# Kernel tuning notes

Hardware: AMD Instinct MI355X
Metric: run time of the kernel (lower is better)

Reference implementation:

```python
import jax, jax.numpy as jnp
from jax import lax
import numpy as np

N, CH_I, CH_H, CH_Q, K, IMSIZE = 128, 2, 150, 10, 16, 64
EPS = 1e-5


def _conv(x, w):
    # 3x3, stride 1, pad 1 == SAME; NCHW / OIHW
    return lax.conv_general_dilated(x, w, (1, 1), 'SAME',
                                    dimension_numbers=('NCHW', 'OIHW', 'NCHW'))


def _maxpool2(x):
    return lax.reduce_window(x, -jnp.inf, lax.max, (1, 1, 2, 2), (1, 1, 2, 2), 'VALID')


def _upsample2(x):
    n, c, h, w = x.shape
    # torch Upsample(scale_factor=2, mode='bilinear', align_corners=False)
    return jax.image.resize(x, (n, c, 2 * h, 2 * w), method='linear')


def _vi_loop(new_r, conv_q_ws, denom):
    # value-iteration recurrence: rv = cat([new_r, v]); q = conv_i(rv); v = max_c q; sum += v
    v0 = jnp.zeros_like(new_r[:, :1])

    def step(carry, w):
        v, s = carry
        rv = jnp.concatenate([new_r, v], axis=1)
        q = _conv(rv, w)
        v = jnp.max(q, axis=1, keepdims=True)
        return (v, s + v), None

    (_, s), _ = lax.scan(step, (v0, v0), conv_q_ws)
    return s / denom


def setup_inputs() -> dict:
    key = jax.random.key(0)
    ks = jax.random.split(key, 12)
    g = lambda k, shp, fan: jax.random.normal(k, shp, dtype=jnp.float32) * (1.0 / np.sqrt(fan))
    X = jax.random.normal(ks[0], (N, CH_I, IMSIZE, IMSIZE), dtype=jnp.float32)
    S1 = jax.random.randint(ks[1], (N,), 0, IMSIZE)
    S2 = jax.random.randint(ks[2], (N,), 0, IMSIZE)
    return {
        'X': X, 'S1': S1, 'S2': S2,
        'conv_h_w': g(ks[3], (CH_H, CH_I, 3, 3), CH_I * 9),
        'conv_r_w': g(ks[4], (1, CH_H, 3, 3), CH_H * 9),
        'conv_q_ws': g(ks[5], (K, CH_Q, 3, 3, 3), 3 * 9),
        'bn_gamma': jnp.ones((CH_Q,), jnp.float32),
        'bn_beta': jnp.zeros((CH_Q,), jnp.float32),
        'duel_w1': g(ks[6], (1, CH_Q), CH_Q),
        'duel_w2': g(ks[7], (8, CH_Q), CH_Q),
        'vi_conv_h_w': g(ks[8], (150, 2, 3, 3), 2 * 9),
        'vi_conv_r_w': g(ks[9], (1, 150, 3, 3), 150 * 9),
        'vi_conv_q_ws': g(ks[10], (16, 10, 2, 3, 3), 2 * 9),
    }


def reference(X, S1, S2, conv_h_w, conv_r_w, conv_q_ws, bn_gamma, bn_beta,
              duel_w1, duel_w2, vi_conv_h_w, vi_conv_r_w, vi_conv_q_ws):
    # --- coarse branch (VImodel on pooled grid) ---
    X1 = _maxpool2(X)                               # [N,2,32,32]
    h1 = _conv(X1, vi_conv_h_w)                     # [N,150,32,32]
    r1 = _conv(h1, vi_conv_r_w)                     # [N,1,32,32]
    v1 = _vi_loop(r1, vi_conv_q_ws, 4.0)            # [N,1,32,32]
    m = _upsample2(v1)                              # [N,1,64,64]
    # --- fine branch ---
    h = _conv(X, conv_h_w)                          # [N,150,64,64]
    r = _conv(h, conv_r_w)                          # [N,1,64,64]
    new_r = jnp.concatenate([m, r], axis=1)         # [N,2,64,64]
    v = _vi_loop(new_r, conv_q_ws, float(K))        # [N,1,64,64]
    rv = jnp.concatenate([new_r, v], axis=1)        # [N,3,64,64]
    q = _conv(rv, conv_q_ws[K - 1])                 # [N,10,64,64]
    # BatchNorm2d (training-mode batch stats, biased variance)
    mean = jnp.mean(q, axis=(0, 2, 3), keepdims=True)
    var = jnp.var(q, axis=(0, 2, 3), keepdims=True)
    q = (q - mean) * jax.lax.rsqrt(var + EPS)
    q = q * bn_gamma[None, :, None, None] + bn_beta[None, :, None, None]
    # attention: q_out[n,c] = q[n, c, S1[n], S2[n]]
    q_out = q[jnp.arange(N), :, S1, S2]             # [N,10]
    # dueling head
    a = jax.nn.relu(q_out @ duel_w1.T)              # [N,1]
    b = jax.nn.relu(q_out @ duel_w2.T)              # [N,8]
    logits = a + (b - jnp.mean(b, axis=1, keepdims=True))
    return logits
```

## Files before the change

kernel.cpp:

```cpp
#include <hip/hip_runtime.h>


#define NEG_BIG (-3.402823466e38f)
#define SCOPE_AGENT __HIP_MEMORY_SCOPE_AGENT
#define WG_SCOPE    __HIP_MEMORY_SCOPE_WORKGROUP
#define CNT_BIG     0x3FFFFFFF

typedef __attribute__((ext_vector_type(8))) short bf16x8;
typedef __attribute__((ext_vector_type(4))) float f32x4;
typedef __attribute__((ext_vector_type(4))) unsigned int u32x4;

__device__ __forceinline__ unsigned f2bf(float f) {
    unsigned u = __builtin_bit_cast(unsigned, f);
    return (u + 0x7FFFu + ((u >> 16) & 1u)) >> 16;
}
__device__ __forceinline__ unsigned pk(float a, float b) {
    return f2bf(a) | (f2bf(b) << 16);
}

__global__ void k_precomp(const float* __restrict__ conv_h_w,
                          const float* __restrict__ conv_r_w,
                          const float* __restrict__ vi_h_w,
                          const float* __restrict__ vi_r_w,
                          const float* __restrict__ conv_q_ws,
                          const float* __restrict__ vi_q_ws,
                          float* __restrict__ ws) {
    __shared__ float sG[2][162];
    int t = threadIdx.x;
    if (t < 324) {
        int set = t / 162;
        int e   = t % 162;
        int ax = e % 3;  int e1 = e / 3;
        int ay = e1 % 3; int e2 = e1 / 3;
        int i  = e2 % 2; int e3 = e2 / 2;
        int bx = e3 % 3; int by = e3 / 3;
        const float* Wh = set ? vi_h_w : conv_h_w;
        const float* Wr = set ? vi_r_w : conv_r_w;
        float acc = 0.f;
        for (int c = 0; c < 150; ++c)
            acc += Wr[(c*3+by)*3+bx] * Wh[((c*2+i)*3+ay)*3+ax];
        sG[set][e] = acc;
        ws[(set ? 320 : 64) + e] = acc;
    }
    if (t >= 480 && t < 512) ws[512 + (t - 480)] = 0.f;
    for (int i = t; i < 8192; i += 1024) ((int*)ws)[4096 + i] = 0;
    {
        int s = t >> 6, lane = t & 63;
        int ch = lane & 15, kb = (lane >> 4) * 8;
        unsigned* dst = (unsigned*)(ws + 81920) + t * 4;
        for (int j = 0; j < 4; ++j) {
            int k0 = kb + 2*j, k1 = k0 + 1;
            float w0 = 0.f, w1 = 0.f;
            if (ch < 10) {
                if (k0 < 27) w0 = conv_q_ws[s*270 + ch*27 + k0];
                if (k1 < 27) w1 = conv_q_ws[s*270 + ch*27 + k1];
            }
            dst[j] = f2bf(w0) | (f2bf(w1) << 16);
        }
    }
    {
        int s = t >> 6, lane = t & 63;
        int ch = lane & 15, kb = (lane >> 4) * 8;
        unsigned* dst = (unsigned*)(ws + 86016) + t * 4;
        for (int j = 0; j < 4; ++j) {
            int k0 = kb + 2*j, k1 = k0 + 1;
            float w0 = 0.f, w1 = 0.f;
            if (ch < 10) {
                if (k0 < 18) w0 = vi_q_ws[s*180 + ch*18 + k0];
                if (k1 < 18) w1 = vi_q_ws[s*180 + ch*18 + k1];
            }
            dst[j] = f2bf(w0) | (f2bf(w1) << 16);
        }
    }
    __syncthreads();
    if (t < 100) {
        int set = t / 50;
        int e   = t % 50;
        int i  = e / 25;
        int oy = (e % 25) / 5;
        int ox = e % 5;
        float acc = 0.f;
        for (int by = 0; by < 3; ++by) {
            int ay = oy - by; if (ay < 0 || ay > 2) continue;
            for (int bx = 0; bx < 3; ++bx) {
                int ax = ox - bx; if (ax < 0 || ax > 2) continue;
                acc += sG[set][(((by*3+bx)*2+i)*3+ay)*3+ax];
            }
        }
        ws[(set ? 256 : 0) + e] = acc;
    }
}

#define SPIN_NB2(M, W, K)                                                     \
  { int sp_ = 0;                                                              \
    for (;;) {                                                                \
      long long both_ = __hip_atomic_load(                                    \
          (const long long*)&M[(W)+1][0], __ATOMIC_ACQUIRE, WG_SCOPE);        \
      if ((int)(both_ & 0xFFFFFFFFll) >= (K) &&                               \
          (int)(both_ >> 32) >= (K)) break;                                   \
      __builtin_amdgcn_s_sleep(1);                                            \
      if (++sp_ > (1 << 20)) break;                                           \
    } }
#define REL_NB2(M, W, K)                                                      \
  if ((t & 63) == 0) {                                                        \
    __hip_atomic_store(&M[(W)+2][0], (K), __ATOMIC_RELEASE, WG_SCOPE);        \
    __hip_atomic_store(&M[(W)][1],   (K), __ATOMIC_RELEASE, WG_SCOPE);        \
  }

#define ITILE(TT)                                                             \
  {                                                                           \
    const int tt_ = (TT);                                                     \
    const int lr  = 4*rpw + (tt_ >> 1);                                       \
    const int px  = (tt_ & 1) * 16 + col;                                     \
    unsigned d0, d1, d2, d3;                                                  \
    if (g == 1) {                                     \
        const unsigned short* vp = &vI[cur][lr][px];                          \
        unsigned w0 = vp[0], w1 = vp[1], w2v = vp[2];                         \
        unsigned w3 = vp[36], w4 = vp[37], w5 = vp[38];                       \
        unsigned w6 = vp[72];                                                 \
        d0 = BsI0[tt_] | (w0 << 16);                                          \
        d1 = w1 | (w2v << 16);                                                \
        d2 = w3 | (w4 << 16);                                                 \
        d3 = w5 | (w6 << 16);                                                 \
    } else if (g == 2) {                             \
        const unsigned short* vp = &vI[cur][lr+2][px+1];                      \
        d0 = (unsigned)vp[0] | (((unsigned)vp[1]) << 16);                     \
        d1 = 0; d2 = 0; d3 = 0;                                               \
    } else if (g == 0) {                                                      \
        d0 = BsI0[tt_]; d1 = BsI1[tt_]; d2 = BsI2[tt_]; d3 = BsI3[tt_];       \
    } else {                                                                  \
        d0 = 0; d1 = 0; d2 = 0; d3 = 0;                                       \
    }                                                                         \
    union { u32x4 u; bf16x8 b; } bv;                                          \
    bv.u = (u32x4){d0, d1, d2, d3};                                           \
    f32x4 d = __builtin_amdgcn_mfma_f32_16x16x32_bf16(                        \
        av.b, bv.b, (f32x4){0.f, 0.f, 0.f, 0.f}, 0, 0, 0);                    \
    float pm01 = fmaxf(d[0], d[1]);                                           \
    float pm4  = fmaxf(pm01, fmaxf(d[2], d[3]));                              \
    float val  = (g < 2) ? pm4 : ((g == 2) ? pm01 : NEG_BIG);                 \
    val = fmaxf(val, __shfl_xor(val, 16));                                    \
    val = fmaxf(val, __shfl_xor(val, 32));                                    \
    vsumI[tt_] += val;                                                        \
    if (lane < 16) vI[nxt][lr + 1][px + 1] = (unsigned short)f2bf(val);       \
  }

#define OTILE(TT)                                                             \
  {                                                                           \
    const int tt_ = (TT);                                                     \
    const int lr  = 2*pp + (tt_ >> 2);                                        \
    const int px  = (tt_ & 3) * 16 + col;                                     \
    unsigned t01 = 0, t23 = 0, t45 = 0, v2 = 0;                               \
    if (g >= 2) {                                                             \
        const unsigned short* vp = &vL[cur][(g == 3) ? (lr + 2) : lr][px];    \
        unsigned v0 = vp[0], v1 = vp[1]; v2 = vp[2];                          \
        unsigned v3 = vp[68], v4 = vp[69], v5 = vp[70];                       \
        t01 = v0 | (v1 << 16);                                                \
        t23 = v2 | (v3 << 16);                                                \
        t45 = v4 | (v5 << 16);                                                \
    }                                                                         \
    union { u32x4 u; bf16x8 b; } bv;                                          \
    bv.u = (u32x4){                                                           \
        (g == 3) ? t01 : Bs0[tt_],                                            \
        (g == 2) ? t01 : ((g == 3) ? v2 : Bs1[tt_]),                          \
        (g == 2) ? t23 : Bs2[tt_],                                            \
        (g == 2) ? t45 : Bs3[tt_]};                                           \
    f32x4 d = __builtin_amdgcn_mfma_f32_16x16x32_bf16(                        \
        av.b, bv.b, (f32x4){0.f, 0.f, 0.f, 0.f}, 0, 0, 0);                    \
    float pm01 = fmaxf(d[0], d[1]);                                           \
    float pm4  = fmaxf(pm01, fmaxf(d[2], d[3]));                              \
    float val  = (g < 2) ? pm4 : ((g == 2) ? pm01 : NEG_BIG);                 \
    val = fmaxf(val, __shfl_xor(val, 16));                                    \
    val = fmaxf(val, __shfl_xor(val, 32));                                    \
    vsum[tt_] += val;                                                         \
    unsigned short vb = (unsigned short)f2bf(val);                            \
    if (lane < 16) vL[nxt][lr + 1][px + 1] = vb;                              \
    const bool btile = half ? (tt_ < 4) : (tt_ >= 4);                         \
    if (K < 15 && rp == 0 && btile && lane < 16)                              \
        ghU[cur * 64 + px] = vb;                 \
  }

__global__
__attribute__((amdgpu_flat_work_group_size(1024, 1024)))
void k_main(
    const float* __restrict__ Xg,
    const int*   __restrict__ S1,
    const int*   __restrict__ S2,
    const float* __restrict__ conv_q_ws,
    const float* __restrict__ vi_q_ws,
    const float* __restrict__ ws,
    float*       __restrict__ wsm)
{
    __shared__ float sX[2][64][64];
    __shared__ float sX1[2][32][32];
    __shared__ float sr1[34][34];
    __shared__ float sm[34][66];
    __shared__ float sr[34][66];
    __shared__ float sVb[34][66];
    __shared__ unsigned short vL[2][35][68];
    __shared__ unsigned short vI[2][34][36];
    __shared__ unsigned int sA [16][64][4];
    __shared__ unsigned int sAI[16][64][4];
    __shared__ float sRed[10][2];
    __shared__ alignas(8) int sMI[10][2];
    __shared__ alignas(8) int sMO[18][2];

    const int bid  = blockIdx.x;
    const int half = (bid >> 3) & 1;
    const int n    = (bid & 7) | ((bid >> 4) << 3);
    const int gr0  = half << 5;
    const int t    = threadIdx.x;
    const int rpw  = t >> 6;
    const int lane = t & 63;
    const int g    = lane >> 4;
    const int col  = lane & 15;

    int*   flagMine = (int*)wsm + 4096 + bid * 32;
    int*   flagPart = (int*)wsm + 4096 + (bid ^ 8) * 32;
    float* ghMine   = wsm + 16384 + bid * 256;
    float* ghPart   = wsm + 16384 + (bid ^ 8) * 256;

    {
        float* z;
        z = &sr1[0][0]; for (int i = t; i < 1156; i += 1024) z[i] = 0.f;
        z = &sm[0][0];  for (int i = t; i < 2244; i += 1024) z[i] = 0.f;
        z = &sr[0][0];  for (int i = t; i < 2244; i += 1024) z[i] = 0.f;
        z = &sVb[0][0]; for (int i = t; i < 2244; i += 1024) z[i] = 0.f;
        unsigned int* zv = (unsigned int*)&vL[0][0][0];
        for (int i = t; i < 2380; i += 1024) zv[i] = 0u;
        unsigned int* zi = (unsigned int*)&vI[0][0][0];
        for (int i = t; i < 1224; i += 1024) zi[i] = 0u;
        if (t < 20) ((float*)sRed)[t] = 0.f;
        if (t < 20)
            ((int*)sMI)[t] = (t == 2 || t == 17) ? CNT_BIG : 0;
        if (t < 36)
            ((int*)sMO)[t] = (t == 2 || t == 33) ? CNT_BIG : 0;
        ((u32x4*)&sA [0][0][0])[t] = ((const u32x4*)(wsm + 81920))[t];
        ((u32x4*)&sAI[0][0][0])[t] = ((const u32x4*)(wsm + 86016))[t];
    }
    {
        const float4* src = (const float4*)(Xg + (size_t)n * 8192);
        float4* dst = (float4*)&sX[0][0][0];
        dst[t] = src[t];
        dst[t + 1024] = src[t + 1024];
    }
    __syncthreads();

    for (int idx = t; idx < 2048; idx += 1024) {
        int c = idx >> 10;
        int y = (idx >> 5) & 31;
        int x = idx & 31;
        float a0 = sX[c][2*y][2*x],   a1 = sX[c][2*y][2*x+1];
        float a2 = sX[c][2*y+1][2*x], a3 = sX[c][2*y+1][2*x+1];
        sX1[c][y][x] = fmaxf(fmaxf(a0, a1), fmaxf(a2, a3));
    }
    __syncthreads();

    if (t < 512) {
        const float* WeffI = ws + 256;
        const float* GI    = ws + 320;
        #pragma unroll
        for (int rep = 0; rep < 2; ++rep) {
            int q  = rep * 64 + lane;
            int iy2 = 4 * rpw + (q >> 5);
            int ix2 = q & 31;
            float acc = 0.f;
            for (int i = 0; i < 2; ++i)
                for (int oy = 0; oy < 5; ++oy) {
                    int yy = iy2 + oy - 2; if (yy < 0 || yy >= 32) continue;
                    for (int ox = 0; ox < 5; ++ox) {
                        int xx = ix2 + ox - 2; if (xx < 0 || xx >= 32) continue;
                        acc += WeffI[i*25 + oy*5 + ox] * sX1[i][yy][xx];
                    }
                }
            if (iy2 == 0 || iy2 == 31 || ix2 == 0 || ix2 == 31) {
                float corr = 0.f;
                for (int by = 0; by < 3; ++by)
                    for (int bx = 0; bx < 3; ++bx) {
                        int qy = iy2 + by - 1, qx = ix2 + bx - 1;
                        if (qy >= 0 && qy < 32 && qx >= 0 && qx < 32) continue;
                        const float* Gb = GI + (by*3+bx)*18;
                        for (int i = 0; i < 2; ++i)
                            for (int ay = 0; ay < 3; ++ay) {
                                int yy2 = qy + ay - 1; if (yy2 < 0 || yy2 >= 32) continue;
                                for (int ax = 0; ax < 3; ++ax) {
                                    int xx2 = qx + ax - 1; if (xx2 < 0 || xx2 >= 32) continue;
                                    corr += Gb[i*9 + ay*3 + ax] * sX1[i][yy2][xx2];
                                }
                            }
                    }
                acc -= corr;
            }
            sr1[1+iy2][1+ix2] = acc;
        }
        REL_NB2(sMI, rpw, 1);
        SPIN_NB2(sMI, rpw, 1);

        unsigned BsI0[8], BsI1[8], BsI2[8], BsI3[8];
        #pragma unroll
        for (int tt = 0; tt < 8; ++tt) {
            const int lr = 4*rpw + (tt >> 1);
            const int px = (tt & 1) * 16 + col;
            unsigned a0 = 0, a1 = 0, a2 = 0, a3 = 0;
            if (g == 0) {
                a0 = pk(sr1[lr][px],     sr1[lr][px+1]);
                a1 = pk(sr1[lr][px+2],   sr1[lr+1][px]);
                a2 = pk(sr1[lr+1][px+1], sr1[lr+1][px+2]);
                a3 = pk(sr1[lr+2][px],   sr1[lr+2][px+1]);
            } else if (g == 1) {
                a0 = f2bf(sr1[lr+2][px+2]);
            }
            BsI0[tt] = a0; BsI1[tt] = a1; BsI2[tt] = a2; BsI3[tt] = a3;
            asm volatile("" : "+v"(BsI0[tt]), "+v"(BsI1[tt]),
                              "+v"(BsI2[tt]), "+v"(BsI3[tt]));
        }
        float vsumI[8] = {0.f, 0.f, 0.f, 0.f, 0.f, 0.f, 0.f, 0.f};
        for (int K = 0; K < 16; ++K) {
            const int cur = K & 1, nxt = cur ^ 1;
            union { u32x4 u; bf16x8 b; } av;
            av.u = *(const u32x4*)&sAI[K][lane][0];
            SPIN_NB2(sMI, rpw, K + 1);
            __builtin_amdgcn_s_setprio(1);
            ITILE(0); ITILE(1); ITILE(2); ITILE(3);
            ITILE(4); ITILE(5); ITILE(6); ITILE(7);
            __builtin_amdgcn_s_setprio(0);
            REL_NB2(sMI, rpw, K + 2);
        }
        #pragma unroll
        for (int tt = 0; tt < 8; ++tt) {
            const int lr = 4*rpw + (tt >> 1);
            const int px = (tt & 1) * 16 + col;
            if (lane < 16) sr1[lr + 1][px + 1] = vsumI[tt] * 0.25f;
        }
    } else {
        const float* WeffO = ws;
        const float* GO    = ws + 64;
        int c = t & 63;
        for (int ar = (t >> 6) - 8; ar < 34; ar += 8) {
            int gg = gr0 + ar - 1;
            if ((unsigned)gg < 64u) {
                float acc = 0.f;
                for (int i = 0; i < 2; ++i)
                    for (int oy = 0; oy < 5; ++oy) {
                        int yy = gg + oy - 2; if (yy < 0 || yy >= 64) continue;
                        for (int ox = 0; ox < 5; ++ox) {
                            int xx = c + ox - 2; if (xx < 0 || xx >= 64) continue;
                            acc += WeffO[i*25 + oy*5 + ox] * sX[i][yy][xx];
                        }
                    }
                if (gg == 0 || gg == 63 || c == 0 || c == 63) {
                    float corr = 0.f;
                    for (int by = 0; by < 3; ++by)
                        for (int bx = 0; bx < 3; ++bx) {
                            int qy = gg + by - 1, qx = c + bx - 1;
                            if (qy >= 0 && qy < 64 && qx >= 0 && qx < 64) continue;
                            const float* Gb = GO + (by*3+bx)*18;
                            for (int i = 0; i < 2; ++i)
                                for (int ay = 0; ay < 3; ++ay) {
                                    int yy2 = qy + ay - 1; if (yy2 < 0 || yy2 >= 64) continue;
                                    for (int ax = 0; ax < 3; ++ax) {
                                        int xx2 = qx + ax - 1; if (xx2 < 0 || xx2 >= 64) continue;
                                        corr += Gb[i*9 + ay*3 + ax] * sX[i][yy2][xx2];
                                    }
                                }
                        }
                    acc -= corr;
                }
                sr[ar][1+c] = acc;
            }
        }
    }
    __syncthreads();

    {
        int c = t & 63;
        for (int ar = t >> 6; ar < 34; ar += 16) {
            int gg = gr0 + ar - 1;
            if ((unsigned)gg < 64u) {
                int y0, y1; float wy0, wy1;
                if ((gg & 1) == 0) { y1 = gg >> 1; y0 = (y1 > 0) ? y1 - 1 : 0; wy1 = 0.75f; wy0 = 0.25f; }
                else               { y0 = gg >> 1; y1 = (y0 < 31) ? y0 + 1 : 31; wy0 = 0.75f; wy1 = 0.25f; }
                int xa, xb; float wx0, wx1;
                if ((c & 1) == 0) { xb = c >> 1; xa = (xb > 0) ? xb - 1 : 0; wx1 = 0.75f; wx0 = 0.25f; }
                else              { xa = c >> 1; xb = (xa < 31) ? xa + 1 : 31; wx0 = 0.75f; wx1 = 0.25f; }
                sm[ar][1+c] = wy0 * (wx0 * sr1[1+y0][1+xa] + wx1 * sr1[1+y0][1+xb])
                            + wy1 * (wx0 * sr1[1+y1][1+xa] + wx1 * sr1[1+y1][1+xb]);
            }
        }
    }
    __syncthreads();

    const int rp   = rpw;
    const int pp   = half ? rp : (15 - rp);
    const int gRowV = half ? 0 : 33;

    unsigned Bs0[8], Bs1[8], Bs2[8], Bs3[8];
    #pragma unroll
    for (int tt = 0; tt < 8; ++tt) {
        const int lr = 2*pp + (tt >> 2);
        const int px = (tt & 3) * 16 + col;
        unsigned a0 = 0, a1 = 0, a2 = 0, a3 = 0;
        if (g == 0) {
            a0 = pk(sm[lr][px],     sm[lr][px+1]);
            a1 = pk(sm[lr][px+2],   sm[lr+1][px]);
            a2 = pk(sm[lr+1][px+1], sm[lr+1][px+2]);
            a3 = pk(sm[lr+2][px],   sm[lr+2][px+1]);
        } else if (g == 1) {
            a0 = pk(sm[lr+2][px+2], sr[lr][px]);
            a1 = pk(sr[lr][px+1],   sr[lr][px+2]);
            a2 = pk(sr[lr+1][px],   sr[lr+1][px+1]);
            a3 = pk(sr[lr+1][px+2], sr[lr+2][px]);
        } else if (g == 2) {
            a0 = pk(sr[lr+2][px+1], sr[lr+2][px+2]);
        }
        Bs0[tt] = a0; Bs1[tt] = a1; Bs2[tt] = a2; Bs3[tt] = a3;
        asm volatile("" : "+v"(Bs0[tt]), "+v"(Bs1[tt]),
                          "+v"(Bs2[tt]), "+v"(Bs3[tt]));
    }

    float vsum[8];
    #pragma unroll
    for (int j = 0; j < 8; ++j) vsum[j] = 0.f;

    unsigned short*       ghU = (unsigned short*)ghMine;
    const unsigned short* gpU = (const unsigned short*)ghPart;

    for (int K = 0; K < 16; ++K) {
        const int cur = K & 1, nxt = cur ^ 1;
        union { u32x4 u; bf16x8 b; } av;
        av.u = *(const u32x4*)&sA[K][lane][0];
        SPIN_NB2(sMO, rp, K);
        __builtin_amdgcn_s_setprio(1);
        if (!half) {
            OTILE(4); OTILE(5); OTILE(6); OTILE(7);
            if (K < 15 && t == 0)
                __hip_atomic_store(flagMine, K + 1, __ATOMIC_RELEASE, SCOPE_AGENT);
            OTILE(0); OTILE(1); OTILE(2); OTILE(3);
        } else {
            OTILE(0); OTILE(1); OTILE(2); OTILE(3);
            if (K < 15 && t == 0)
                __hip_atomic_store(flagMine, K + 1, __ATOMIC_RELEASE, SCOPE_AGENT);
            OTILE(4); OTILE(5); OTILE(6); OTILE(7);
        }
        __builtin_amdgcn_s_setprio(0);
        REL_NB2(sMO, rp, K + 1);
        if (K < 15 && rp == 0) {
            if (t == 0) {
                int spins = 0;
                while (__hip_atomic_load(flagPart, __ATOMIC_ACQUIRE, SCOPE_AGENT) < K + 1) {
                    __builtin_amdgcn_s_sleep(1);
                    if (++spins > (1 << 23)) break;
                }
            }
            vL[nxt][gRowV][lane + 1] = gpU[cur * 64 + lane];
        }
    }
    __syncthreads();

    #pragma unroll
    for (int tt = 0; tt < 8; ++tt) {
        const int lr = 2*pp + (tt >> 2);
        const int px = (tt & 3) * 16 + col;
        if (lane < 16) sVb[lr + 1][px + 1] = vsum[tt];
    }
    if (rp == 0) {
        const int bAr = half ? 1 : 32;
        const int gAr = half ? 0 : 33;
        float sv = sVb[bAr][1 + lane];
        __hip_atomic_store(ghMine + 128 + lane, sv, __ATOMIC_RELAXED, SCOPE_AGENT);
        if (t == 0) {
            __hip_atomic_store(flagMine, 16, __ATOMIC_RELEASE, SCOPE_AGENT);
            int spins = 0;
            while (__hip_atomic_load(flagPart, __ATOMIC_ACQUIRE, SCOPE_AGENT) < 16) {
                __builtin_amdgcn_s_sleep(1);
                if (++spins > (1 << 23)) break;
            }
        }
        sVb[gAr][1 + lane] =
            __hip_atomic_load(ghPart + 128 + lane, __ATOMIC_RELAXED, SCOPE_AGENT);
    }
    __syncthreads();

    {
        const float* wk = conv_q_ws + 15 * 270;
        const int oc = lane;
        float pm[4][3], pq[4][3], pv[4][3];
        #pragma unroll
        for (int dy = 0; dy < 4; ++dy)
            #pragma unroll
            for (int dx = 0; dx < 3; ++dx) {
                pm[dy][dx] = sm[2*pp+dy][oc+dx];
                pq[dy][dx] = sr[2*pp+dy][oc+dx];
                pv[dy][dx] = sVb[2*pp+dy][oc+dx] * 0.0625f;
            }
        int sy = S1[n], sx = S2[n];
        int ry0 = gr0 + 2*pp, ry1 = ry0 + 1;
        float* qpix = wsm + 544 + n * 10;
        #pragma unroll
        for (int ch = 0; ch < 10; ++ch) {
            const float* wc = wk + ch * 27;
            float q0 = 0.f, q1 = 0.f;
            #pragma unroll
            for (int ky = 0; ky < 3; ++ky)
                #pragma unroll
                for (int kx = 0; kx < 3; ++kx) {
                    float wm = wc[ky*3+kx];
                    float wr = wc[9  + ky*3+kx];
                    float wv = wc[18 + ky*3+kx];
                    q0 += wm * pm[ky][kx]   + wr * pq[ky][kx]   + wv * pv[ky][kx];
                    q1 += wm * pm[ky+1][kx] + wr * pq[ky+1][kx] + wv * pv[ky+1][kx];
                }
            if (oc == sx) {
                if (ry0 == sy) qpix[ch] = q0;
                if (ry1 == sy) qpix[ch] = q1;
            }
            float ls = q0 + q1, lq = q0*q0 + q1*q1;
            #pragma unroll
            for (int off = 32; off > 0; off >>= 1) {
                ls += __shfl_down(ls, off);
                lq += __shfl_down(lq, off);
            }
            if ((t & 63) == 0) {
                atomicAdd(&sRed[ch][0], ls);
                atomicAdd(&sRed[ch][1], lq);
            }
        }
        __syncthreads();
        if (t < 10) {
            atomicAdd(wsm + 512 + t, sRed[t][0]);
            atomicAdd(wsm + 528 + t, sRed[t][1]);
        }
    }
}

__global__ void k_final(const float* __restrict__ ws,
                        const float* __restrict__ gamma,
                        const float* __restrict__ beta,
                        const float* __restrict__ w1,
                        const float* __restrict__ w2,
                        float* __restrict__ out) {
    int n = threadIdx.x;
    if (n >= 128) return;
    const float inv = 1.f / 524288.f;
    float qn[10];
    for (int c = 0; c < 10; ++c) {
        float mean = ws[512 + c] * inv;
        float var  = ws[528 + c] * inv - mean * mean;
        float q    = ws[544 + n * 10 + c];
        qn[c] = (q - mean) * rsqrtf(var + 1e-5f) * gamma[c] + beta[c];
    }
    float a = 0.f;
    for (int c = 0; c < 10; ++c) a += qn[c] * w1[c];
    a = fmaxf(a, 0.f);
    float b[8], mb = 0.f;
    for (int j = 0; j < 8; ++j) {
        float bj = 0.f;
        for (int c = 0; c < 10; ++c) bj += qn[c] * w2[j * 10 + c];
        bj = fmaxf(bj, 0.f);
        b[j] = bj;
        mb += bj;
    }
    mb *= 0.125f;
    for (int j = 0; j < 8; ++j) out[n * 8 + j] = a + b[j] - mb;
}

extern "C" void kernel_launch(void* const* d_in, const int* in_sizes, int n_in,
                              void* d_out, int out_size, void* d_ws, size_t ws_size,
                              hipStream_t stream) {
    const float* X         = (const float*)d_in[0];
    const int*   S1        = (const int*)  d_in[1];
    const int*   S2        = (const int*)  d_in[2];
    const float* conv_h_w  = (const float*)d_in[3];
    const float* conv_r_w  = (const float*)d_in[4];
    const float* conv_q_ws = (const float*)d_in[5];
    const float* bn_gamma  = (const float*)d_in[6];
    const float* bn_beta   = (const float*)d_in[7];
    const float* duel_w1   = (const float*)d_in[8];
    const float* duel_w2   = (const float*)d_in[9];
    const float* vi_h_w    = (const float*)d_in[10];
    const float* vi_r_w    = (const float*)d_in[11];
    const float* vi_q_ws   = (const float*)d_in[12];
    float* ws = (float*)d_ws;

    k_precomp<<<1, 1024, 0, stream>>>(conv_h_w, conv_r_w, vi_h_w, vi_r_w,
                                      conv_q_ws, vi_q_ws, ws);
    k_main<<<256, 1024, 0, stream>>>(X, S1, S2, conv_q_ws, vi_q_ws, ws, ws);
    k_final<<<1, 128, 0, stream>>>(ws, bn_gamma, bn_beta, duel_w1, duel_w2,
                                   (float*)d_out);
}
```

Baseline: 168.8 us.

## Split each image into four row-quarter blocks with neighbor halo exchange

The main kernel now runs 512 blocks of 512 threads instead of 256 blocks of 1024. Each image is split into four 16-row quarters rather than two 32-row halves, and each quarter trades halo rows with the blocks above and below through global-memory flags every value-iteration step. The coarse branch is computed redundantly per block and run in sequence rather than on warp-specialised halves. MFMA weights are read straight from global instead of being staged in LDS. The aim is more parallelism and lower per-block LDS use, at the cost of more inter-block synchronisation, duplicated coarse work and a risk of spin deadlock if blocks are not co-resident.

```diff
diff --git a/kernel.cpp b/kernel.cpp
--- a/kernel.cpp
+++ b/kernel.cpp
@@ -43,11 +43,11 @@
         ws[(set ? 320 : 64) + e] = acc;
     }
     if (t >= 480 && t < 512) ws[512 + (t - 480)] = 0.f;
-    for (int i = t; i < 8192; i += 1024) ((int*)ws)[4096 + i] = 0;
+    for (int i = t; i < 32768; i += 1024) ((int*)ws)[4096 + i] = 0;
     {
         int s = t >> 6, lane = t & 63;
         int ch = lane & 15, kb = (lane >> 4) * 8;
-        unsigned* dst = (unsigned*)(ws + 81920) + t * 4;
+        unsigned* dst = (unsigned*)(ws + 172032) + t * 4;
         for (int j = 0; j < 4; ++j) {
             int k0 = kb + 2*j, k1 = k0 + 1;
             float w0 = 0.f, w1 = 0.f;
@@ -61,7 +61,7 @@
     {
         int s = t >> 6, lane = t & 63;
         int ch = lane & 15, kb = (lane >> 4) * 8;
-        unsigned* dst = (unsigned*)(ws + 86016) + t * 4;
+        unsigned* dst = (unsigned*)(ws + 176128) + t * 4;
         for (int j = 0; j < 4; ++j) {
             int k0 = kb + 2*j, k1 = k0 + 1;
             float w0 = 0.f, w1 = 0.f;
@@ -144,7 +144,7 @@
     if (lane < 16) vI[nxt][lr + 1][px + 1] = (unsigned short)f2bf(val);       \
   }
 
-#define OTILE(TT)                                                             \
+#define OTILE_H(TT, HD)                                                       \
   {                                                                           \
     const int tt_ = (TT);                                                     \
     const int lr  = 2*pp + (tt_ >> 2);                                        \
@@ -174,13 +174,14 @@
     vsum[tt_] += val;                                                         \
     unsigned short vb = (unsigned short)f2bf(val);                            \
     if (lane < 16) vL[nxt][lr + 1][px + 1] = vb;                              \
-    const bool btile = half ? (tt_ < 4) : (tt_ >= 4);                         \
-    if (K < 15 && rp == 0 && btile && lane < 16)                              \
-        ghU[cur * 64 + px] = vb;                 \
+    if ((HD) == 1 && K < 15 && q > 0 && lane < 16)                            \
+        myD16[cur * 64 + px] = vb;                                            \
+    if ((HD) == 2 && K < 15 && q < 3 && lane < 16)                            \
+        myU16[cur * 64 + px] = vb;                                            \
   }
 
 __global__
-__attribute__((amdgpu_flat_work_group_size(1024, 1024)))
+__attribute__((amdgpu_flat_work_group_size(512, 512)))
 void k_main(
     const float* __restrict__ Xg,
     const int*   __restrict__ S1,
@@ -193,59 +194,60 @@
     __shared__ float sX[2][64][64];
     __shared__ float sX1[2][32][32];
     __shared__ float sr1[34][34];
-    __shared__ float sm[34][66];
-    __shared__ float sr[34][66];
-    __shared__ float sVb[34][66];
-    __shared__ unsigned short vL[2][35][68];
+    __shared__ float sm[18][66];
+    __shared__ float sr[18][66];
+    __shared__ float sVb[18][66];
+    __shared__ unsigned short vL[2][19][68];
     __shared__ unsigned short vI[2][34][36];
-    __shared__ unsigned int sA [16][64][4];
-    __shared__ unsigned int sAI[16][64][4];
     __shared__ float sRed[10][2];
     __shared__ alignas(8) int sMI[10][2];
-    __shared__ alignas(8) int sMO[18][2];
+    __shared__ alignas(8) int sMO[10][2];
 
     const int bid  = blockIdx.x;
-    const int half = (bid >> 3) & 1;
-    const int n    = (bid & 7) | ((bid >> 4) << 3);
-    const int gr0  = half << 5;
+    const int n    = bid & 127;
+    const int q    = bid >> 7;
+    const int qr0  = q << 4;
     const int t    = threadIdx.x;
     const int rpw  = t >> 6;
     const int lane = t & 63;
     const int g    = lane >> 4;
     const int col  = lane & 15;
 
-    int*   flagMine = (int*)wsm + 4096 + bid * 32;
-    int*   flagPart = (int*)wsm + 4096 + (bid ^ 8) * 32;
-    float* ghMine   = wsm + 16384 + bid * 256;
-    float* ghPart   = wsm + 16384 + (bid ^ 8) * 256;
+    int* flgBase = (int*)wsm + 4096;
+    int* flgU = flgBase + (bid * 2 + 0) * 32;
+    int* flgD = flgBase + (bid * 2 + 1) * 32;
+    float* hal = wsm + 40960 + bid * 256;
+    unsigned short* myU16 = (unsigned short*)hal;
+    unsigned short* myD16 = (unsigned short*)hal + 128;
 
     {
         float* z;
-        z = &sr1[0][0]; for (int i = t; i < 1156; i += 1024) z[i] = 0.f;
-        z = &sm[0][0];  for (int i = t; i < 2244; i += 1024) z[i] = 0.f;
-        z = &sr[0][0];  for (int i = t; i < 2244; i += 1024) z[i] = 0.f;
-        z = &sVb[0][0]; for (int i = t; i < 2244; i += 1024) z[i] = 0.f;
+        z = &sr1[0][0]; for (int i = t; i < 1156; i += 512) z[i] = 0.f;
+        z = &sm[0][0];  for (int i = t; i < 1188; i += 512) z[i] = 0.f;
+        z = &sr[0][0];  for (int i = t; i < 1188; i += 512) z[i] = 0.f;
+        z = &sVb[0][0]; for (int i = t; i < 1188; i += 512) z[i] = 0.f;
         unsigned int* zv = (unsigned int*)&vL[0][0][0];
-        for (int i = t; i < 2380; i += 1024) zv[i] = 0u;
+        for (int i = t; i < 1292; i += 512) zv[i] = 0u;
         unsigned int* zi = (unsigned int*)&vI[0][0][0];
-        for (int i = t; i < 1224; i += 1024) zi[i] = 0u;
+        for (int i = t; i < 1224; i += 512) zi[i] = 0u;
         if (t < 20) ((float*)sRed)[t] = 0.f;
-        if (t < 20)
-            ((int*)sMI)[t] = (t == 2 || t == 17) ? CNT_BIG : 0;
-        if (t < 36)
-            ((int*)sMO)[t] = (t == 2 || t == 33) ? CNT_BIG : 0;
-        ((u32x4*)&sA [0][0][0])[t] = ((const u32x4*)(wsm + 81920))[t];
-        ((u32x4*)&sAI[0][0][0])[t] = ((const u32x4*)(wsm + 86016))[t];
+        if (t < 20) ((int*)sMI)[t] = (t == 2 || t == 17) ? CNT_BIG : 0;
+        if (t >= 20 && t < 40) {
+            int u = t - 20;
+            ((int*)sMO)[u] = (u == 2 || u == 17) ? CNT_BIG : 0;
+        }
     }
     {
         const float4* src = (const float4*)(Xg + (size_t)n * 8192);
         float4* dst = (float4*)&sX[0][0][0];
         dst[t] = src[t];
+        dst[t + 512]  = src[t + 512];
         dst[t + 1024] = src[t + 1024];
-    }
-    __syncthreads();
-
-    for (int idx = t; idx < 2048; idx += 1024) {
+        dst[t + 1536] = src[t + 1536];
+    }
+    __syncthreads();
+
+    for (int idx = t; idx < 2048; idx += 512) {
         int c = idx >> 10;
         int y = (idx >> 5) & 31;
         int x = idx & 31;
@@ -255,14 +257,13 @@
     }
     __syncthreads();
 
-    if (t < 512) {
+    {
         const float* WeffI = ws + 256;
         const float* GI    = ws + 320;
         #pragma unroll
         for (int rep = 0; rep < 2; ++rep) {
-            int q  = rep * 64 + lane;
-            int iy2 = 4 * rpw + (q >> 5);
-            int ix2 = q & 31;
+            int p   = rep * 512 + t;
+            int iy2 = p >> 5, ix2 = p & 31;
             float acc = 0.f;
             for (int i = 0; i < 2; ++i)
                 for (int oy = 0; oy < 5; ++oy) {
@@ -292,9 +293,10 @@
             }
             sr1[1+iy2][1+ix2] = acc;
         }
-        REL_NB2(sMI, rpw, 1);
-        SPIN_NB2(sMI, rpw, 1);
-
+    }
+    __syncthreads();
+
+    {
         unsigned BsI0[8], BsI1[8], BsI2[8], BsI3[8];
         #pragma unroll
         for (int tt = 0; tt < 8; ++tt) {
@@ -317,13 +319,13 @@
         for (int K = 0; K < 16; ++K) {
             const int cur = K & 1, nxt = cur ^ 1;
             union { u32x4 u; bf16x8 b; } av;
-            av.u = *(const u32x4*)&sAI[K][lane][0];
-            SPIN_NB2(sMI, rpw, K + 1);
+            av.u = ((const u32x4*)(wsm + 176128))[K * 64 + lane];
+            SPIN_NB2(sMI, rpw, K);
             __builtin_amdgcn_s_setprio(1);
             ITILE(0); ITILE(1); ITILE(2); ITILE(3);
             ITILE(4); ITILE(5); ITILE(6); ITILE(7);
             __builtin_amdgcn_s_setprio(0);
-            REL_NB2(sMI, rpw, K + 2);
+            REL_NB2(sMI, rpw, K + 1);
         }
         #pragma unroll
         for (int tt = 0; tt < 8; ++tt) {
@@ -331,13 +333,24 @@
             const int px = (tt & 1) * 16 + col;
             if (lane < 16) sr1[lr + 1][px + 1] = vsumI[tt] * 0.25f;
         }
-    } else {
+    }
+    __syncthreads();
+
+    {
         const float* WeffO = ws;
         const float* GO    = ws + 64;
-        int c = t & 63;
-        for (int ar = (t >> 6) - 8; ar < 34; ar += 8) {
-            int gg = gr0 + ar - 1;
+        int c = lane;
+        for (int ar = rpw; ar < 18; ar += 8) {
+            int gg = qr0 + ar - 1;
             if ((unsigned)gg < 64u) {
+                int y0, y1; float wy0, wy1;
+                if ((gg & 1) == 0) { y1 = gg >> 1; y0 = (y1 > 0) ? y1 - 1 : 0; wy1 = 0.75f; wy0 = 0.25f; }
+                else               { y0 = gg >> 1; y1 = (y0 < 31) ? y0 + 1 : 31; wy0 = 0.75f; wy1 = 0.25f; }
+                int xa, xb; float wx0, wx1;
+                if ((c & 1) == 0) { xb = c >> 1; xa = (xb > 0) ? xb - 1 : 0; wx1 = 0.75f; wx0 = 0.25f; }
+                else              { xa = c >> 1; xb = (xa < 31) ? xa + 1 : 31; wx0 = 0.75f; wx1 = 0.25f; }
+                sm[ar][1+c] = wy0 * (wx0 * sr1[1+y0][1+xa] + wx1 * sr1[1+y0][1+xb])
+                            + wy1 * (wx0 * sr1[1+y1][1+xa] + wx1 * sr1[1+y1][1+xb]);
                 float acc = 0.f;
                 for (int i = 0; i < 2; ++i)
                     for (int oy = 0; oy < 5; ++oy) {
@@ -371,27 +384,7 @@
     }
     __syncthreads();
 
-    {
-        int c = t & 63;
-        for (int ar = t >> 6; ar < 34; ar += 16) {
-            int gg = gr0 + ar - 1;
-            if ((unsigned)gg < 64u) {
-                int y0, y1; float wy0, wy1;
-                if ((gg & 1) == 0) { y1 = gg >> 1; y0 = (y1 > 0) ? y1 - 1 : 0; wy1 = 0.75f; wy0 = 0.25f; }
-                else               { y0 = gg >> 1; y1 = (y0 < 31) ? y0 + 1 : 31; wy0 = 0.75f; wy1 = 0.25f; }
-                int xa, xb; float wx0, wx1;
-                if ((c & 1) == 0) { xb = c >> 1; xa = (xb > 0) ? xb - 1 : 0; wx1 = 0.75f; wx0 = 0.25f; }
-                else              { xa = c >> 1; xb = (xa < 31) ? xa + 1 : 31; wx0 = 0.75f; wx1 = 0.25f; }
-                sm[ar][1+c] = wy0 * (wx0 * sr1[1+y0][1+xa] + wx1 * sr1[1+y0][1+xb])
-                            + wy1 * (wx0 * sr1[1+y1][1+xa] + wx1 * sr1[1+y1][1+xb]);
-            }
-        }
-    }
-    __syncthreads();
-
-    const int rp   = rpw;
-    const int pp   = half ? rp : (15 - rp);
-    const int gRowV = half ? 0 : 33;
+    const int pp = rpw;
 
     unsigned Bs0[8], Bs1[8], Bs2[8], Bs3[8];
     #pragma unroll
@@ -421,37 +414,57 @@
     #pragma unroll
     for (int j = 0; j < 8; ++j) vsum[j] = 0.f;
 
-    unsigned short*       ghU = (unsigned short*)ghMine;
-    const unsigned short* gpU = (const unsigned short*)ghPart;
-
     for (int K = 0; K < 16; ++K) {
         const int cur = K & 1, nxt = cur ^ 1;
         union { u32x4 u; bf16x8 b; } av;
-        av.u = *(const u32x4*)&sA[K][lane][0];
-        SPIN_NB2(sMO, rp, K);
+        av.u = ((const u32x4*)(wsm + 172032))[K * 64 + lane];
+        SPIN_NB2(sMO, rpw, K);
         __builtin_amdgcn_s_setprio(1);
-        if (!half) {
-            OTILE(4); OTILE(5); OTILE(6); OTILE(7);
-            if (K < 15 && t == 0)
-                __hip_atomic_store(flagMine, K + 1, __ATOMIC_RELEASE, SCOPE_AGENT);
-            OTILE(0); OTILE(1); OTILE(2); OTILE(3);
+        if (rpw == 0) {
+            OTILE_H(0, 1); OTILE_H(1, 1); OTILE_H(2, 1); OTILE_H(3, 1);
+            if (K < 15 && q > 0 && lane == 0)
+                __hip_atomic_store(flgD, K + 1, __ATOMIC_RELEASE, SCOPE_AGENT);
+            OTILE_H(4, 0); OTILE_H(5, 0); OTILE_H(6, 0); OTILE_H(7, 0);
+            __builtin_amdgcn_s_setprio(0);
+            REL_NB2(sMO, rpw, K + 1);
+            if (K < 15 && q > 0) {
+                const int* bU = flgBase + ((bid - 128) * 2 + 0) * 32;
+                if (lane == 0) {
+                    int spins = 0;
+                    while (__hip_atomic_load(bU, __ATOMIC_ACQUIRE, SCOPE_AGENT) < K + 1) {
+                        __builtin_amdgcn_s_sleep(1);
+                        if (++spins > (1 << 23)) break;
+                    }
+                }
+                const unsigned short* nb =
+                    (const unsigned short*)(wsm + 40960 + (bid - 128) * 256);
+                vL[nxt][0][lane + 1] = nb[cur * 64 + lane];
+            }
+        } else if (rpw == 7) {
+            OTILE_H(4, 2); OTILE_H(5, 2); OTILE_H(6, 2); OTILE_H(7, 2);
+            if (K < 15 && q < 3 && lane == 0)
+                __hip_atomic_store(flgU, K + 1, __ATOMIC_RELEASE, SCOPE_AGENT);
+            OTILE_H(0, 0); OTILE_H(1, 0); OTILE_H(2, 0); OTILE_H(3, 0);
+            __builtin_amdgcn_s_setprio(0);
+            REL_NB2(sMO, rpw, K + 1);
+            if (K < 15 && q < 3) {
+                const int* aD = flgBase + ((bid + 128) * 2 + 1) * 32;
+                if (lane == 0) {
+                    int spins = 0;
+                    while (__hip_atomic_load(aD, __ATOMIC_ACQUIRE, SCOPE_AGENT) < K + 1) {
+                        __builtin_amdgcn_s_sleep(1);
+                        if (++spins > (1 << 23)) break;
+                    }
+                }
+                const unsigned short* nb =
+                    (const unsigned short*)(wsm + 40960 + (bid + 128) * 256) + 128;
+                vL[nxt][17][lane + 1] = nb[cur * 64 + lane];
+            }
         } else {
-            OTILE(0); OTILE(1); OTILE(2); OTILE(3);
-            if (K < 15 && t == 0)
-                __hip_atomic_store(flagMine, K + 1, __ATOMIC_RELEASE, SCOPE_AGENT);
-            OTILE(4); OTILE(5); OTILE(6); OTILE(7);
-        }
-        __builtin_amdgcn_s_setprio(0);
-        REL_NB2(sMO, rp, K + 1);
-        if (K < 15 && rp == 0) {
-            if (t == 0) {
-                int spins = 0;
-                while (__hip_atomic_load(flagPart, __ATOMIC_ACQUIRE, SCOPE_AGENT) < K + 1) {
-                    __builtin_amdgcn_s_sleep(1);
-                    if (++spins > (1 << 23)) break;
-                }
-            }
-            vL[nxt][gRowV][lane + 1] = gpU[cur * 64 + lane];
+            OTILE_H(0, 0); OTILE_H(1, 0); OTILE_H(2, 0); OTILE_H(3, 0);
+            OTILE_H(4, 0); OTILE_H(5, 0); OTILE_H(6, 0); OTILE_H(7, 0);
+            __builtin_amdgcn_s_setprio(0);
+            REL_NB2(sMO, rpw, K + 1);
         }
     }
     __syncthreads();
@@ -462,21 +475,31 @@
         const int px = (tt & 3) * 16 + col;
         if (lane < 16) sVb[lr + 1][px + 1] = vsum[tt];
     }
-    if (rp == 0) {
-        const int bAr = half ? 1 : 32;
-        const int gAr = half ? 0 : 33;
-        float sv = sVb[bAr][1 + lane];
-        __hip_atomic_store(ghMine + 128 + lane, sv, __ATOMIC_RELAXED, SCOPE_AGENT);
-        if (t == 0) {
-            __hip_atomic_store(flagMine, 16, __ATOMIC_RELEASE, SCOPE_AGENT);
+    if (rpw == 0 && q > 0) {
+        hal[192 + lane] = sVb[1][1 + lane];
+        if (lane == 0) {
+            __hip_atomic_store(flgD, 16, __ATOMIC_RELEASE, SCOPE_AGENT);
+            const int* bU = flgBase + ((bid - 128) * 2 + 0) * 32;
             int spins = 0;
-            while (__hip_atomic_load(flagPart, __ATOMIC_ACQUIRE, SCOPE_AGENT) < 16) {
+            while (__hip_atomic_load(bU, __ATOMIC_ACQUIRE, SCOPE_AGENT) < 16) {
                 __builtin_amdgcn_s_sleep(1);
                 if (++spins > (1 << 23)) break;
             }
         }
-        sVb[gAr][1 + lane] =
-            __hip_atomic_load(ghPart + 128 + lane, __ATOMIC_RELAXED, SCOPE_AGENT);
+        sVb[0][1 + lane] = *(wsm + 40960 + (bid - 128) * 256 + 128 + lane);
+    }
+    if (rpw == 7 && q < 3) {
+        hal[128 + lane] = sVb[16][1 + lane];
+        if (lane == 0) {
+            __hip_atomic_store(flgU, 16, __ATOMIC_RELEASE, SCOPE_AGENT);
+            const int* aD = flgBase + ((bid + 128) * 2 + 1) * 32;
+            int spins = 0;
+            while (__hip_atomic_load(aD, __ATOMIC_ACQUIRE, SCOPE_AGENT) < 16) {
+                __builtin_amdgcn_s_sleep(1);
+                if (++spins > (1 << 23)) break;
+            }
+        }
+        sVb[17][1 + lane] = *(wsm + 40960 + (bid + 128) * 256 + 192 + lane);
     }
     __syncthreads();
 
@@ -493,7 +516,7 @@
                 pv[dy][dx] = sVb[2*pp+dy][oc+dx] * 0.0625f;
             }
         int sy = S1[n], sx = S2[n];
-        int ry0 = gr0 + 2*pp, ry1 = ry0 + 1;
+        int ry0 = qr0 + 2*pp, ry1 = ry0 + 1;
         float* qpix = wsm + 544 + n * 10;
         #pragma unroll
         for (int ch = 0; ch < 10; ++ch) {
@@ -583,7 +606,7 @@
 
     k_precomp<<<1, 1024, 0, stream>>>(conv_h_w, conv_r_w, vi_h_w, vi_r_w,
                                       conv_q_ws, vi_q_ws, ws);
-    k_main<<<256, 1024, 0, stream>>>(X, S1, S2, conv_q_ws, vi_q_ws, ws, ws);
+    k_main<<<512, 512, 0, stream>>>(X, S1, S2, conv_q_ws, vi_q_ws, ws, ws);
     k_final<<<1, 128, 0, stream>>>(ws, bn_gamma, bn_beta, duel_w1, duel_w2,
                                    (float*)d_out);
 }
```

New measurement: 383.7 us. 127% more time.
